# Kernel tuning notes

Measured on AMD Instinct MI355X. Metric: run time of the kernel, lower is better.

## Reference

```python
import jax, jax.numpy as jnp
import numpy as np

TEMPERATURE = 0.5
BATCH_SIZE = 4096
EPS = 1e-8  # torch.nn.CosineSimilarity default eps


def setup_inputs() -> dict:
    key = jax.random.key(0)
    k1, k2 = jax.random.split(key)
    z1 = jax.random.normal(k1, (BATCH_SIZE, 256), dtype=jnp.float32)
    z2 = jax.random.normal(k2, (BATCH_SIZE, 256), dtype=jnp.float32)
    return {"z1": z1, "z2": z2}


def reference(z1, z2):
    B = z1.shape[0]
    N = 2 * B
    reps = jnp.concatenate([z1, z2], axis=0)  # [N, D]
    # Cosine similarity (torch clamps each norm to eps before dividing)
    norms = jnp.maximum(jnp.linalg.norm(reps, axis=1, keepdims=True), EPS)
    z = reps / norms
    sim = z @ z.T  # [N, N] cosine similarity matrix

    # positives: diagonals at offsets +B and -B (they are identical by symmetry,
    # but keep the original concat order: [diag(+B), diag(-B)])
    l_pos = jnp.diagonal(sim, offset=B)
    r_pos = jnp.diagonal(sim, offset=-B)
    positives = jnp.concatenate([l_pos, r_pos])  # [N]

    inv_t = 1.0 / TEMPERATURE
    pos_logit = positives * inv_t  # logits[:, 0]

    # negatives are all off-diagonal entries of each row (the positive pair is
    # thus present twice in the logits, faithful to the original). CE with
    # label 0 => loss_i = logsumexp(logits_i) - logits_i[0].
    neg_logits = jnp.where(jnp.eye(N, dtype=bool), -jnp.inf, sim * inv_t)
    lse = jnp.logaddexp(pos_logit, jax.scipy.special.logsumexp(neg_logits, axis=1))
    loss = jnp.sum(lse - pos_logit) / N
    return loss
```

## Files before the change

kernel.cpp:

```cpp
#include <hip/hip_runtime.h>
#include <hip/hip_bf16.h>
#include <cstdint>
#include <cstddef>
#include <math.h>

#define BSZ   4096
#define NROW  8192
#define DIM   256
#define INV_T 2.0f
#define EPS_N 1e-8f

typedef __attribute__((ext_vector_type(4))) float f32x4;

__device__ __forceinline__ void load_lds16(const void* g, void* l) {
    __builtin_amdgcn_global_load_lds(
        (const __attribute__((address_space(1))) void*)g,
        (__attribute__((address_space(3))) void*)l,
        16, 0, 0);
}

#define VMWAIT(N) asm volatile("s_waitcnt vmcnt(" #N ")" ::: "memory")

__global__ __launch_bounds__(256)
void nt_normalize(const float* __restrict__ z1,
                  const float* __restrict__ z2,
                  char* __restrict__ zn3,
                  unsigned int* __restrict__ cnt) {
    const int wave = threadIdx.x >> 6;
    const int lane = threadIdx.x & 63;
    const int row  = blockIdx.x * 4 + wave;
    const float* src = (row < BSZ) ? (z1 + (size_t)row * DIM)
                                   : (z2 + (size_t)(row - BSZ) * DIM);
    const float4 v = ((const float4*)src)[lane];
    float ss = v.x * v.x + v.y * v.y + v.z * v.z + v.w * v.w;
    #pragma unroll
    for (int off = 32; off; off >>= 1) ss += __shfl_xor(ss, off);
    const float rinv = 1.0f / fmaxf(sqrtf(ss), EPS_N);
    int pk = 0;
    pk = __builtin_amdgcn_cvt_pk_fp8_f32(v.x * rinv, v.y * rinv, pk, false);
    pk = __builtin_amdgcn_cvt_pk_fp8_f32(v.z * rinv, v.w * rinv, pk, true);
    const int s    = row >> 7;
    const int lrow = row & 127;
    const int kc   = lane >> 4;
    const int unit = (lane >> 1) & 7;
    const int off4 = (lane & 1) * 4;
    const int u    = unit ^ (lrow & 7);
    *(int*)(zn3 + (size_t)s * 32768 + kc * 8192 + lrow * 64 + u * 8 + off4) = pk;
    if (row == 0 && lane == 0) *cnt = 0;
}

__global__ __launch_bounds__(256)
void nt_gram(const char* __restrict__ zn3,
             float* __restrict__ part,
             float* __restrict__ pos) {
    const int l = blockIdx.x;
    int bi = (int)((129.0 - sqrt(16641.0 - 8.0 * (double)l)) * 0.5);
    while (64 * (bi + 1) - (bi + 1) * bi / 2 <= l) ++bi;
    while (64 * bi - bi * (bi - 1) / 2 > l) --bi;
    const int bj = bi + (l - (64 * bi - bi * (bi - 1) / 2));

    __shared__ char lds[32768];

    const int t    = threadIdx.x;
    const int lane = t & 63;
    const int wave = t >> 6;
    const int wrow = (wave >> 1) * 64;
    const int wcol = (wave & 1) * 64;
    const int q    = lane >> 4;
    const int r16  = lane & 15;
    const int sw   = r16 & 7;
    const int t16  = t * 16;

    const char* A2 = zn3 + (size_t)bi * 32768;
    const char* B2 = zn3 + (size_t)bj * 32768;

    f32x4 acc[4][4] = {};

#define STAGE(kc, buf)                                                   \
    {                                                                    \
        char* d_ = lds + (buf) * 16384;                                  \
        load_lds16(A2 + (kc) * 8192 + t16,        d_ + t16);             \
        load_lds16(A2 + (kc) * 8192 + 4096 + t16, d_ + 4096 + t16);      \
        load_lds16(B2 + (kc) * 8192 + t16,        d_ + 8192 + t16);      \
        load_lds16(B2 + (kc) * 8192 + 4096 + t16, d_ + 12288 + t16);     \
    }

#define COMPUTE(buf)                                                     \
    {                                                                    \
        const char* As_ = lds + (buf) * 16384;                           \
        const char* Bs_ = As_ + 8192;                                    \
        _Pragma("unroll")                                                \
        for (int kh = 0; kh < 2; ++kh) {                                 \
            const int spos = (((kh << 2) + q) ^ sw) << 3;                \
            long af[4], bfv[4];                                          \
            _Pragma("unroll")                                            \
            for (int mi = 0; mi < 4; ++mi)                               \
                af[mi] = *(const long*)(As_ + (wrow + mi * 16 + r16) * 64 + spos); \
            _Pragma("unroll")                                            \
            for (int ni = 0; ni < 4; ++ni)                               \
                bfv[ni] = *(const long*)(Bs_ + (wcol + ni * 16 + r16) * 64 + spos); \
            _Pragma("unroll")                                            \
            for (int mi = 0; mi < 4; ++mi)                               \
                _Pragma("unroll")                                        \
                for (int ni = 0; ni < 4; ++ni)                           \
                    acc[mi][ni] = __builtin_amdgcn_mfma_f32_16x16x32_fp8_fp8( \
                        af[mi], bfv[ni], acc[mi][ni], 0, 0, 0);          \
        }                                                                \
    }

    STAGE(0, 0)
    STAGE(1, 1)
    VMWAIT(4);
    __builtin_amdgcn_s_barrier();
    COMPUTE(0)
    __builtin_amdgcn_s_barrier();
    __builtin_amdgcn_sched_barrier(0);
    STAGE(2, 0)
    VMWAIT(4);
    __builtin_amdgcn_s_barrier();
    COMPUTE(1)
    __builtin_amdgcn_s_barrier();
    __builtin_amdgcn_sched_barrier(0);
    STAGE(3, 1)
    VMWAIT(4);
    __builtin_amdgcn_s_barrier();
    COMPUTE(0)
    VMWAIT(0);
    __builtin_amdgcn_s_barrier();
    COMPUTE(1)
#undef STAGE
#undef COMPUTE

    const int c = r16;
    const bool diag_block = (bi == bj);
    const int rslot = 2 * bj + (wcol >> 6);
    const int cslot = 2 * bi + (wrow >> 6);
    float colp[4] = {0.f, 0.f, 0.f, 0.f};

    #pragma unroll
    for (int mi = 0; mi < 4; ++mi) {
        #pragma unroll
        for (int r = 0; r < 4; ++r) {
            const int grow = bi * 128 + wrow + mi * 16 + q * 4 + r;
            float s = 0.f;
            #pragma unroll
            for (int ni = 0; ni < 4; ++ni) {
                const int gcol = bj * 128 + wcol + ni * 16 + c;
                const float val = acc[mi][ni][r];
                float e = __expf(val * INV_T);
                e = (grow == gcol) ? 0.f : e;
                s += e;
                colp[ni] += e;
                if (gcol == grow + BSZ) {
                    pos[grow] = val;
                    pos[gcol] = val;
                }
            }
            s += __shfl_xor(s, 1);
            s += __shfl_xor(s, 2);
            s += __shfl_xor(s, 4);
            s += __shfl_xor(s, 8);
            if (c == 0) part[(size_t)grow * 128 + rslot] = s;
        }
    }
    if (!diag_block) {
        #pragma unroll
        for (int ni = 0; ni < 4; ++ni) {
            float cs = colp[ni];
            cs += __shfl_xor(cs, 16);
            cs += __shfl_xor(cs, 32);
            if (q == 0)
                part[(size_t)(bj * 128 + wcol + ni * 16 + c) * 128 + cslot] = cs;
        }
    }
}

__global__ __launch_bounds__(256)
void nt_finalize(const float* __restrict__ part,
                 const float* __restrict__ pos,
                 float* __restrict__ blocksum,
                 unsigned int* __restrict__ cnt,
                 float* __restrict__ out) {
    const int b    = blockIdx.x;
    const int t    = threadIdx.x;
    const int lane = t & 63;
    const int row  = b * 128 + (t >> 1);
    const int half = t & 1;

    const float4* p4 = (const float4*)(part + (size_t)row * 128 + half * 64);
    float s = 0.f;
    #pragma unroll
    for (int j = 0; j < 16; ++j) {
        const float4 v = p4[j];
        s += v.x + v.y + v.z + v.w;
    }
    s += __shfl_xor(s, 1);
    float contrib = 0.f;
    if (half == 0) {
        const float pl = pos[row] * INV_T;
        contrib = logf(__expf(pl) + s) - pl;
    }
    #pragma unroll
    for (int off = 32; off; off >>= 1) contrib += __shfl_xor(contrib, off);
    __shared__ float r4[4];
    __shared__ int   slast;
    if (lane == 0) r4[t >> 6] = contrib;
    __syncthreads();
    if (t == 0) {
        blocksum[b] = r4[0] + r4[1] + r4[2] + r4[3];
        __threadfence();
        slast = (atomicAdd(cnt, 1u) == 63u);
    }
    __syncthreads();
    if (slast && t < 64) {
        float v = atomicAdd(&blocksum[t], 0.0f);
        #pragma unroll
        for (int off = 32; off; off >>= 1) v += __shfl_xor(v, off);
        if (t == 0) out[0] = v * (1.0f / NROW);
    }
}

extern "C" void kernel_launch(void* const* d_in, const int* in_sizes, int n_in,
                              void* d_out, int out_size, void* d_ws, size_t ws_size,
                              hipStream_t stream) {
    const float* z1 = (const float*)d_in[0];
    const float* z2 = (const float*)d_in[1];
    float* out = (float*)d_out;

    char*  zn3      = (char*)d_ws;
    float* part     = (float*)((char*)d_ws + (size_t)2097152);
    float* pos      = (float*)((char*)d_ws + (size_t)6291456);
    float* blocksum = pos + NROW;
    unsigned int* cnt = (unsigned int*)(blocksum + 64);

    nt_normalize<<<NROW / 4, 256, 0, stream>>>(z1, z2, zn3, cnt);
    nt_gram<<<2080, 256, 0, stream>>>(zn3, part, pos);
    nt_finalize<<<64, 256, 0, stream>>>(part, pos, blocksum, cnt, out);
}
```

Before: 95.07 us.

## Merge pairs of row-block tiles into 256x128 workgroups sharing the B tile

```diff
diff --git a/kernel.cpp b/kernel.cpp
--- a/kernel.cpp
+++ b/kernel.cpp
@@ -49,17 +49,17 @@
     if (row == 0 && lane == 0) *cnt = 0;
 }
 
-__global__ __launch_bounds__(256)
+__global__ __launch_bounds__(512)
 void nt_gram(const char* __restrict__ zn3,
              float* __restrict__ part,
              float* __restrict__ pos) {
-    const int l = blockIdx.x;
-    int bi = (int)((129.0 - sqrt(16641.0 - 8.0 * (double)l)) * 0.5);
-    while (64 * (bi + 1) - (bi + 1) * bi / 2 <= l) ++bi;
-    while (64 * bi - bi * (bi - 1) / 2 > l) --bi;
-    const int bj = bi + (l - (64 * bi - bi * (bi - 1) / 2));
-
-    __shared__ char lds[32768];
+    const int p = blockIdx.x;
+    int I = (int)((65.0 - sqrt(4225.0 - 4.0 * (double)p)) * 0.5);
+    while ((I + 1) * (65 - (I + 1)) <= p) ++I;
+    while (I * (65 - I) > p) --I;
+    const int j = 2 * I + (p - I * (65 - I));
+
+    __shared__ char lds[49152];
 
     const int t    = threadIdx.x;
     const int lane = t & 63;
@@ -70,35 +70,37 @@
     const int r16  = lane & 15;
     const int sw   = r16 & 7;
     const int t16  = t * 16;
-
-    const char* A2 = zn3 + (size_t)bi * 32768;
-    const char* B2 = zn3 + (size_t)bj * 32768;
+    const int ahalf = (wrow >> 7) * 8192;
+    const int lw    = wrow & 64;
+
+    const char* Ah0  = zn3 + (size_t)(2 * I) * 32768;
+    const char* Ah1  = zn3 + (size_t)(2 * I + 1) * 32768;
+    const char* Bsrc = zn3 + (size_t)j * 32768;
 
     f32x4 acc[4][4] = {};
 
 #define STAGE(kc, buf)                                                   \
     {                                                                    \
-        char* d_ = lds + (buf) * 16384;                                  \
-        load_lds16(A2 + (kc) * 8192 + t16,        d_ + t16);             \
-        load_lds16(A2 + (kc) * 8192 + 4096 + t16, d_ + 4096 + t16);      \
-        load_lds16(B2 + (kc) * 8192 + t16,        d_ + 8192 + t16);      \
-        load_lds16(B2 + (kc) * 8192 + 4096 + t16, d_ + 12288 + t16);     \
+        char* d_ = lds + (buf) * 24576;                                  \
+        load_lds16(Ah0 + (kc) * 8192 + t16,  d_ + t16);                  \
+        load_lds16(Ah1 + (kc) * 8192 + t16,  d_ + 8192 + t16);           \
+        load_lds16(Bsrc + (kc) * 8192 + t16, d_ + 16384 + t16);          \
     }
 
 #define COMPUTE(buf)                                                     \
     {                                                                    \
-        const char* As_ = lds + (buf) * 16384;                           \
-        const char* Bs_ = As_ + 8192;                                    \
+        const char* Aw = lds + (buf) * 24576 + ahalf;                    \
+        const char* Bw = lds + (buf) * 24576 + 16384;                    \
         _Pragma("unroll")                                                \
         for (int kh = 0; kh < 2; ++kh) {                                 \
             const int spos = (((kh << 2) + q) ^ sw) << 3;                \
             long af[4], bfv[4];                                          \
             _Pragma("unroll")                                            \
             for (int mi = 0; mi < 4; ++mi)                               \
-                af[mi] = *(const long*)(As_ + (wrow + mi * 16 + r16) * 64 + spos); \
+                af[mi] = *(const long*)(Aw + (lw + mi * 16 + r16) * 64 + spos); \
             _Pragma("unroll")                                            \
             for (int ni = 0; ni < 4; ++ni)                               \
-                bfv[ni] = *(const long*)(Bs_ + (wcol + ni * 16 + r16) * 64 + spos); \
+                bfv[ni] = *(const long*)(Bw + (wcol + ni * 16 + r16) * 64 + spos); \
             _Pragma("unroll")                                            \
             for (int mi = 0; mi < 4; ++mi)                               \
                 _Pragma("unroll")                                        \
@@ -110,19 +112,19 @@
 
     STAGE(0, 0)
     STAGE(1, 1)
-    VMWAIT(4);
+    VMWAIT(3);
     __builtin_amdgcn_s_barrier();
     COMPUTE(0)
     __builtin_amdgcn_s_barrier();
     __builtin_amdgcn_sched_barrier(0);
     STAGE(2, 0)
-    VMWAIT(4);
+    VMWAIT(3);
     __builtin_amdgcn_s_barrier();
     COMPUTE(1)
     __builtin_amdgcn_s_barrier();
     __builtin_amdgcn_sched_barrier(0);
     STAGE(3, 1)
-    VMWAIT(4);
+    VMWAIT(3);
     __builtin_amdgcn_s_barrier();
     COMPUTE(0)
     VMWAIT(0);
@@ -131,46 +133,50 @@
 #undef STAGE
 #undef COMPUTE
 
-    const int c = r16;
-    const bool diag_block = (bi == bj);
-    const int rslot = 2 * bj + (wcol >> 6);
-    const int cslot = 2 * bi + (wrow >> 6);
+    const int  bi_w = 2 * I + (wrow >> 7);
+    const bool skip = (bi_w > j);
+    const bool diag = (bi_w == j);
+    const int  c     = r16;
+    const int  rslot = 2 * j + (wcol >> 6);
+    const int  cslot = 2 * bi_w + (lw >> 6);
     float colp[4] = {0.f, 0.f, 0.f, 0.f};
 
-    #pragma unroll
-    for (int mi = 0; mi < 4; ++mi) {
+    if (!skip) {
         #pragma unroll
-        for (int r = 0; r < 4; ++r) {
-            const int grow = bi * 128 + wrow + mi * 16 + q * 4 + r;
-            float s = 0.f;
+        for (int mi = 0; mi < 4; ++mi) {
+            #pragma unroll
+            for (int r = 0; r < 4; ++r) {
+                const int grow = bi_w * 128 + lw + mi * 16 + q * 4 + r;
+                float s = 0.f;
+                #pragma unroll
+                for (int ni = 0; ni < 4; ++ni) {
+                    const int gcol = j * 128 + wcol + ni * 16 + c;
+                    const float val = acc[mi][ni][r];
+                    float e = __expf(val * INV_T);
+                    e = (grow == gcol) ? 0.f : e;
+                    s += e;
+                    colp[ni] += e;
+                    if (gcol == grow + BSZ) {
+                        pos[grow] = val;
+                        pos[gcol] = val;
+                    }
+                }
+                s += __shfl_xor(s, 1);
+                s += __shfl_xor(s, 2);
+                s += __shfl_xor(s, 4);
+                s += __shfl_xor(s, 8);
+                if (c == 0) part[(size_t)grow * 128 + rslot] = s;
+            }
+        }
+        if (!diag) {
             #pragma unroll
             for (int ni = 0; ni < 4; ++ni) {
-                const int gcol = bj * 128 + wcol + ni * 16 + c;
-                const float val = acc[mi][ni][r];
-                float e = __expf(val * INV_T);
-                e = (grow == gcol) ? 0.f : e;
-                s += e;
-                colp[ni] += e;
-                if (gcol == grow + BSZ) {
-                    pos[grow] = val;
-                    pos[gcol] = val;
-                }
+                float cs = colp[ni];
+                cs += __shfl_xor(cs, 16);
+                cs += __shfl_xor(cs, 32);
+                if (q == 0)
+                    part[(size_t)(j * 128 + wcol + ni * 16 + c) * 128 + cslot] = cs;
             }
-            s += __shfl_xor(s, 1);
-            s += __shfl_xor(s, 2);
-            s += __shfl_xor(s, 4);
-            s += __shfl_xor(s, 8);
-            if (c == 0) part[(size_t)grow * 128 + rslot] = s;
-        }
-    }
-    if (!diag_block) {
-        #pragma unroll
-        for (int ni = 0; ni < 4; ++ni) {
-            float cs = colp[ni];
-            cs += __shfl_xor(cs, 16);
-            cs += __shfl_xor(cs, 32);
-            if (q == 0)
-                part[(size_t)(bj * 128 + wcol + ni * 16 + c) * 128 + cslot] = cs;
         }
     }
 }
@@ -234,6 +240,6 @@
     unsigned int* cnt = (unsigned int*)(blocksum + 64);
 
     nt_normalize<<<NROW / 4, 256, 0, stream>>>(z1, z2, zn3, cnt);
-    nt_gram<<<2080, 256, 0, stream>>>(zn3, part, pos);
+    nt_gram<<<1056, 512, 0, stream>>>(zn3, part, pos);
     nt_finalize<<<64, 256, 0, stream>>>(part, pos, blocksum, cnt, out);
 }
```

After: 95.51 us. No clear change (+0.5%).

## Fuse finalize reduction into gram kernel via last-arriving-block tickets

Applied to the files above, without the earlier changes.

```diff
diff --git a/kernel.cpp b/kernel.cpp
--- a/kernel.cpp
+++ b/kernel.cpp
@@ -9,6 +9,8 @@
 #define DIM   256
 #define INV_T 2.0f
 #define EPS_N 1e-8f
+#define NTILE 2080
+#define NFIN  64
 
 typedef __attribute__((ext_vector_type(4))) float f32x4;
 
@@ -46,13 +48,16 @@
     const int off4 = (lane & 1) * 4;
     const int u    = unit ^ (lrow & 7);
     *(int*)(zn3 + (size_t)s * 32768 + kc * 8192 + lrow * 64 + u * 8 + off4) = pk;
-    if (row == 0 && lane == 0) *cnt = 0;
+    if (row == 0 && lane == 0) { cnt[0] = 0u; cnt[1] = 0u; }
 }
 
 __global__ __launch_bounds__(256)
 void nt_gram(const char* __restrict__ zn3,
              float* __restrict__ part,
-             float* __restrict__ pos) {
+             float* __restrict__ pos,
+             float* __restrict__ blocksum,
+             unsigned int* __restrict__ cnt,
+             float* __restrict__ out) {
     const int l = blockIdx.x;
     int bi = (int)((129.0 - sqrt(16641.0 - 8.0 * (double)l)) * 0.5);
     while (64 * (bi + 1) - (bi + 1) * bi / 2 <= l) ++bi;
@@ -173,50 +178,62 @@
                 part[(size_t)(bj * 128 + wcol + ni * 16 + c) * 128 + cslot] = cs;
         }
     }
-}
-
-__global__ __launch_bounds__(256)
-void nt_finalize(const float* __restrict__ part,
-                 const float* __restrict__ pos,
-                 float* __restrict__ blocksum,
-                 unsigned int* __restrict__ cnt,
-                 float* __restrict__ out) {
-    const int b    = blockIdx.x;
-    const int t    = threadIdx.x;
-    const int lane = t & 63;
-    const int row  = b * 128 + (t >> 1);
-    const int half = t & 1;
-
-    const float4* p4 = (const float4*)(part + (size_t)row * 128 + half * 64);
-    float s = 0.f;
-    #pragma unroll
-    for (int j = 0; j < 16; ++j) {
-        const float4 v = p4[j];
-        s += v.x + v.y + v.z + v.w;
-    }
-    s += __shfl_xor(s, 1);
-    float contrib = 0.f;
-    if (half == 0) {
-        const float pl = pos[row] * INV_T;
-        contrib = logf(__expf(pl) + s) - pl;
-    }
-    #pragma unroll
-    for (int off = 32; off; off >>= 1) contrib += __shfl_xor(contrib, off);
-    __shared__ float r4[4];
-    __shared__ int   slast;
-    if (lane == 0) r4[t >> 6] = contrib;
+
+    unsigned int* ltk = (unsigned int*)lds;
+    float*        r4  = (float*)lds + 16;
+    int*          win = (int*)lds + 24;
     __syncthreads();
     if (t == 0) {
-        blocksum[b] = r4[0] + r4[1] + r4[2] + r4[3];
         __threadfence();
-        slast = (atomicAdd(cnt, 1u) == 63u);
+        ltk[0] = atomicAdd(&cnt[0], 1u);
     }
     __syncthreads();
-    if (slast && t < 64) {
-        float v = atomicAdd(&blocksum[t], 0.0f);
-        #pragma unroll
-        for (int off = 32; off; off >>= 1) v += __shfl_xor(v, off);
-        if (t == 0) out[0] = v * (1.0f / NROW);
+    const unsigned int ticket = ltk[0];
+    if (ticket >= NTILE - NFIN) {
+        const int chunk = (int)ticket - (NTILE - NFIN);
+        if (t == 0) {
+            while (__hip_atomic_load(&cnt[0], __ATOMIC_ACQUIRE,
+                                     __HIP_MEMORY_SCOPE_AGENT) < NTILE)
+                __builtin_amdgcn_s_sleep(4);
+        }
+        __syncthreads();
+        const int row  = chunk * 128 + (t >> 1);
+        const int half = t & 1;
+        const unsigned long long* p8 =
+            (const unsigned long long*)(part + (size_t)row * 128 + half * 64);
+        float s = 0.f;
+        #pragma unroll
+        for (int j2 = 0; j2 < 32; ++j2) {
+            const unsigned long long w = __hip_atomic_load(
+                &p8[j2], __ATOMIC_RELAXED, __HIP_MEMORY_SCOPE_AGENT);
+            const float2 f2 = __builtin_bit_cast(float2, w);
+            s += f2.x + f2.y;
+        }
+        s += __shfl_xor(s, 1);
+        float contrib = 0.f;
+        if (half == 0) {
+            const float pv = __hip_atomic_load(
+                &pos[row], __ATOMIC_RELAXED, __HIP_MEMORY_SCOPE_AGENT);
+            const float pl = pv * INV_T;
+            contrib = logf(__expf(pl) + s) - pl;
+        }
+        #pragma unroll
+        for (int off = 32; off; off >>= 1) contrib += __shfl_xor(contrib, off);
+        if (lane == 0) r4[wave] = contrib;
+        __syncthreads();
+        if (t == 0) {
+            blocksum[chunk] = r4[0] + r4[1] + r4[2] + r4[3];
+            __threadfence();
+            win[0] = (atomicAdd(&cnt[1], 1u) == NFIN - 1u);
+        }
+        __syncthreads();
+        if (win[0] && t < 64) {
+            float v = __hip_atomic_load(&blocksum[t], __ATOMIC_RELAXED,
+                                        __HIP_MEMORY_SCOPE_AGENT);
+            #pragma unroll
+            for (int off = 32; off; off >>= 1) v += __shfl_xor(v, off);
+            if (t == 0) out[0] = v * (1.0f / NROW);
+        }
     }
 }
 
@@ -234,6 +251,5 @@
     unsigned int* cnt = (unsigned int*)(blocksum + 64);
 
     nt_normalize<<<NROW / 4, 256, 0, stream>>>(z1, z2, zn3, cnt);
-    nt_gram<<<2080, 256, 0, stream>>>(zn3, part, pos);
-    nt_finalize<<<64, 256, 0, stream>>>(part, pos, blocksum, cnt, out);
-}
+    nt_gram<<<NTILE, 256, 0, stream>>>(zn3, part, pos, blocksum, cnt, out);
+}
```

Measured after the change: 176.3 us. 1.85x slower.
